# Optimization experiments

Hardware: AMD Instinct MI355X
Metric: run time of the kernel (lower is better)

Reference implementation:

```python
import jax, jax.numpy as jnp
import numpy as np

N = 100000
E = 3200000
F_IN = 256
F_OUT = 256
HID = 64


def setup_inputs() -> dict:
    key = jax.random.key(0)
    ks = jax.random.split(key, 16)
    stdv = 1.0 / np.sqrt(F_OUT)
    std_att = 1.0 / np.sqrt(HID)
    std_att_vec = 1.0 / np.sqrt(3.0)
    u = lambda k, shape, s: jax.random.uniform(k, shape, jnp.float32, -s, s)
    return {
        "inputx": jax.random.normal(ks[0], (N, F_IN), jnp.float32),
        "row_A": jax.random.randint(ks[1], (E,), 0, N),
        "col_A": jax.random.randint(ks[2], (E,), 0, N),
        "val_A": jax.random.uniform(ks[3], (E,), jnp.float32),
        "row_A2": jax.random.randint(ks[4], (E,), 0, N),
        "col_A2": jax.random.randint(ks[5], (E,), 0, N),
        "val_A2": jax.random.uniform(ks[6], (E,), jnp.float32),
        "weight_A": u(ks[7], (F_IN, F_OUT), stdv),
        "weight_A2": u(ks[8], (F_IN, F_OUT), stdv),
        "weight_mlp": u(ks[9], (F_IN, F_OUT), stdv),
        "W_k0": u(ks[10], (F_OUT, HID), std_att),
        "W_k1": u(ks[11], (F_OUT, HID), std_att),
        "W_k2": u(ks[12], (F_OUT, HID), std_att),
        "att_vec_A": u(ks[13], (F_OUT, HID), std_att),
        "att_vec_A2": u(ks[14], (F_OUT, HID), std_att),
        "att_vec_mlp": u(ks[15], (F_OUT, HID), std_att),
        "att_vec": u(jax.random.fold_in(key, 99), (3, 3), std_att_vec),
    }


def _spmm(row, col, val, x, n):
    # COO sparse-dense matmul: out[r] += val_e * x[c]
    return jax.ops.segment_sum(val[:, None] * x[col], row, num_segments=n)


def reference(inputx, row_A, col_A, val_A, row_A2, col_A2, val_A2,
              weight_A, weight_A2, weight_mlp, W_k0, W_k1, W_k2,
              att_vec_A, att_vec_A2, att_vec_mlp, att_vec):
    n = inputx.shape[0]
    out_A = jax.nn.relu(_spmm(row_A, col_A, val_A, inputx @ weight_A, n))
    out_A2 = jax.nn.relu(_spmm(row_A2, col_A2, val_A2, inputx @ weight_A2, n))
    out_mlp = jax.nn.relu(inputx @ weight_mlp)
    # attention gating
    T = 3.0
    k0 = jnp.mean(out_A @ W_k0, axis=0, keepdims=True)    # [1, HID]
    k1 = jnp.mean(out_A2 @ W_k1, axis=0, keepdims=True)
    k2 = jnp.mean(out_mlp @ W_k2, axis=0, keepdims=True)
    logits = jnp.concatenate([
        (out_A @ att_vec_A) @ k0.T,      # [N, 1]
        (out_A2 @ att_vec_A2) @ k1.T,
        (out_mlp @ att_vec_mlp) @ k2.T,
    ], axis=1)                           # [N, 3]
    att = jax.nn.softmax((jax.nn.sigmoid(logits) @ att_vec) / T, axis=1)
    return 3.0 * (att[:, 0:1] * out_A + att[:, 1:2] * out_A2 + att[:, 2:3] * out_mlp)
```

## Files before the change

### kernel.cpp

```cpp
#include <hip/hip_runtime.h>

typedef __bf16 bf16;
typedef __bf16 bf16x4 __attribute__((ext_vector_type(4)));
typedef __bf16 bf16x8 __attribute__((ext_vector_type(8)));
typedef float f32x4 __attribute__((ext_vector_type(4)));

__device__ __forceinline__ f32x4 bf2f(bf16x4 v){
  f32x4 r; r[0]=(float)v[0]; r[1]=(float)v[1]; r[2]=(float)v[2]; r[3]=(float)v[3]; return r;
}

#define NBMAX 1600
#define NBP   1601
#define CHUNK 16384

__global__ __launch_bounds__(256) void k_xcvt(const float* __restrict__ X, bf16* __restrict__ Xb, int total){
  int i = (blockIdx.x*256 + threadIdx.x)*8;
  if (i + 8 <= total){
    float4 a = *(const float4*)(X+i);
    float4 b = *(const float4*)(X+i+4);
    bf16x8 v;
    v[0]=(bf16)a.x; v[1]=(bf16)a.y; v[2]=(bf16)a.z; v[3]=(bf16)a.w;
    v[4]=(bf16)b.x; v[5]=(bf16)b.y; v[6]=(bf16)b.z; v[7]=(bf16)b.w;
    *(bf16x8*)(Xb+i) = v;
  }
}

__global__ __launch_bounds__(256) void k_wt(const float* __restrict__ W0, const float* __restrict__ W1,
                                            const float* __restrict__ W2, bf16* __restrict__ WT3){
  int n = blockIdx.x, mat = blockIdx.y, k = threadIdx.x;
  const float* W = (mat==0)?W0:((mat==1)?W1:W2);
  WT3[mat*65536 + n*256 + k] = (bf16)W[k*256 + n];
}

__global__ __launch_bounds__(512) void k_gemm(const bf16* __restrict__ Xb, const bf16* __restrict__ WT3,
        bf16* __restrict__ O0, bf16* __restrict__ O1, bf16* __restrict__ O2,
        float* __restrict__ colsum, int N){
  __shared__ __align__(16) bf16 sA[128*32];
  __shared__ __align__(16) bf16 sB[256*32];
  __shared__ float gcs[256];
  int t = threadIdx.x;
  int lane = t & 63, wave = t>>6, wm = wave>>2, wn = wave&3;
  int mat = blockIdx.y;
  int m0 = blockIdx.x*128;
  const bf16* WT = WT3 + mat*65536;
  bf16* OUT = (mat==0)?O0:((mat==1)?O1:O2);

  f32x4 acc[4][4];
#pragma unroll
  for (int i=0;i<4;i++)
#pragma unroll
    for (int j=0;j<4;j++){ acc[i][j][0]=0.f; acc[i][j][1]=0.f; acc[i][j][2]=0.f; acc[i][j][3]=0.f; }

  int ar = t>>2, ac = t&3;
  int alc = ac ^ ((ar>>1)&3);
  int agrow = m0 + ar; if (agrow > N-1) agrow = N-1;
  const bf16* gA = Xb + (size_t)agrow*256 + alc*8;
  bf16* lA = sA + ar*32 + ac*8;

  int br = t>>2, bc = t&3;
  int blc = bc ^ ((br>>1)&3);
  const bf16* gB0 = WT + br*256 + blc*8;
  const bf16* gB1 = WT + (br+128)*256 + blc*8;
  bf16* lB0 = sB + br*32 + bc*8;
  bf16* lB1 = sB + (br+128)*32 + bc*8;

  for (int k0=0; k0<256; k0+=32){
    __syncthreads();
    *(bf16x8*)lA  = *(const bf16x8*)(gA  + k0);
    *(bf16x8*)lB0 = *(const bf16x8*)(gB0 + k0);
    *(bf16x8*)lB1 = *(const bf16x8*)(gB1 + k0);
    __syncthreads();

    bf16x8 af[4], bfr[4];
#pragma unroll
    for (int i=0;i<4;i++){
      int arow = wm*64 + i*16 + (lane&15);
      int pc = (lane>>4) ^ ((arow>>1)&3);
      af[i] = *(const bf16x8*)(sA + arow*32 + pc*8);
    }
#pragma unroll
    for (int j=0;j<4;j++){
      int brow = wn*64 + j*16 + (lane&15);
      int pc = (lane>>4) ^ ((brow>>1)&3);
      bfr[j] = *(const bf16x8*)(sB + brow*32 + pc*8);
    }
#pragma unroll
    for (int i=0;i<4;i++)
#pragma unroll
      for (int j=0;j<4;j++)
        acc[i][j] = __builtin_amdgcn_mfma_f32_16x16x32_bf16(af[i], bfr[j], acc[i][j], 0,0,0);
  }

  int col0 = wn*64 + (lane&15);
  int rb = m0 + wm*64 + ((lane>>4)<<2);
  bool isrelu = (mat==2);
  float pj[4] = {0.f,0.f,0.f,0.f};
#pragma unroll
  for (int i=0;i<4;i++){
#pragma unroll
    for (int tt=0; tt<4; tt++){
      int r = rb + i*16 + tt;
      if (r < N){
#pragma unroll
        for (int j=0;j<4;j++){
          float vv = acc[i][j][tt];
          if (isrelu && vv < 0.f) vv = 0.f;
          if (isrelu) pj[j] += vv;
          OUT[(size_t)r*256 + col0 + j*16] = (bf16)vv;
        }
      }
    }
  }
  if (isrelu){
    if (t < 256) gcs[t] = 0.f;
    __syncthreads();
#pragma unroll
    for (int j=0;j<4;j++) atomicAdd(&gcs[col0 + j*16], pj[j]);
    __syncthreads();
    if (t < 256) atomicAdd(&colsum[512 + t], gcs[t]);
  }
}

__global__ __launch_bounds__(512) void k_bcnt(const int* __restrict__ rowA, const int* __restrict__ rowA2,
    int* __restrict__ bcnt, int E, int NB){
  __shared__ int hist[NBMAX];
  int mat = blockIdx.y;
  const int* row = mat? rowA2 : rowA;
  int t = threadIdx.x;
  for (int i=t; i<NB; i+=512) hist[i] = 0;
  __syncthreads();
  int base = blockIdx.x * CHUNK;
  int endi = base + CHUNK; if (endi > E) endi = E;
  for (int i = base + t; i < endi; i += 512) atomicAdd(&hist[row[i] >> 6], 1);
  __syncthreads();
  for (int i=t; i<NB; i+=512){
    int c = hist[i];
    if (c) atomicAdd(&bcnt[mat*NBMAX + i], c);
  }
}

__global__ __launch_bounds__(256) void k_bscan(const int* __restrict__ bcnt, int* __restrict__ gstart,
    int* __restrict__ gcur, int NB, int E){
  __shared__ int ss[256];
  __shared__ int carry;
  int mat = blockIdx.x;
  int t = threadIdx.x;
  if (t==0) carry = 0;
  __syncthreads();
  for (int base=0; base<NB; base+=256){
    int i = base + t;
    int v = (i < NB) ? bcnt[mat*NBMAX + i] : 0;
    ss[t] = v; __syncthreads();
    for (int off=1; off<256; off<<=1){
      int u = (t>=off)? ss[t-off] : 0;
      __syncthreads();
      ss[t] += u;
      __syncthreads();
    }
    int excl = carry + ss[t] - v;
    if (i < NB){ gstart[mat*NBP + i] = excl; gcur[mat*NB + i] = excl; }
    int tot = ss[255];
    __syncthreads();
    if (t==0) carry += tot;
    __syncthreads();
  }
  if (t==0) gstart[mat*NBP + NB] = E;
}

__global__ __launch_bounds__(512) void k_binT(const int* __restrict__ rowA, const int* __restrict__ colA,
    const float* __restrict__ valA, const int* __restrict__ rowA2, const int* __restrict__ colA2,
    const float* __restrict__ valA2, int* __restrict__ gcur,
    int2* __restrict__ pTA, int2* __restrict__ pTA2, int E, int NB){
  __shared__ int hist[NBMAX];
  int mat = blockIdx.y;
  const int* row = mat? rowA2 : rowA;
  const int* col = mat? colA2 : colA;
  const float* val = mat? valA2 : valA;
  int2* pT = mat? pTA2 : pTA;
  int t = threadIdx.x;
  for (int i=t; i<NB; i+=512) hist[i] = 0;
  __syncthreads();
  int base = blockIdx.x * CHUNK;
  int endi = base + CHUNK; if (endi > E) endi = E;
  for (int i = base + t; i < endi; i += 512) atomicAdd(&hist[row[i] >> 6], 1);
  __syncthreads();
  for (int i=t; i<NB; i+=512){
    int c = hist[i];
    if (c) hist[i] = atomicAdd(&gcur[mat*NB + i], c);
  }
  __syncthreads();
  for (int i = base + t; i < endi; i += 512){
    int r = row[i];
    int pos = atomicAdd(&hist[r >> 6], 1);
    int2 p; p.x = ((r & 63) << 17) | col[i]; p.y = __float_as_int(val[i]);
    pT[pos] = p;
  }
}

__global__ __launch_bounds__(256) void k_csr(const int2* __restrict__ pTA, const int2* __restrict__ pTA2,
    const int* __restrict__ gstart, int* __restrict__ rsA, int* __restrict__ rsA2,
    int2* __restrict__ permA, int2* __restrict__ permA2, int N, int NB, int E){
  __shared__ int rowst[64];
  __shared__ int fill[64];
  int mat = blockIdx.y;
  const int2* pT = mat? pTA2 : pTA;
  int2* perm = mat? permA2 : permA;
  int* rs = mat? rsA2 : rsA;
  int b = blockIdx.x;
  int t = threadIdx.x;
  int r0 = b*64;
  int start = gstart[mat*NBP + b];
  int end   = gstart[mat*NBP + b + 1];
  if (t < 64) fill[t] = 0;
  __syncthreads();
  for (int i = start + t; i < end; i += 256) atomicAdd(&fill[pT[i].x >> 17], 1);
  __syncthreads();
  if (t < 64){
    int v = fill[t];
    int x = v;
#pragma unroll
    for (int off=1; off<64; off<<=1){
      int u = __shfl_up(x, off, 64);
      if (t >= off) x += u;
    }
    int st = start + x - v;
    rowst[t] = st;
    if (r0 + t < N) rs[r0 + t] = st;
    fill[t] = 0;
  }
  __syncthreads();
  for (int i = start + t; i < end; i += 256){
    int2 e = pT[i];
    int rl = e.x >> 17;
    int pos = atomicAdd(&fill[rl], 1);
    int2 o; o.x = e.x & 0x1FFFF; o.y = e.y;
    perm[rowst[rl] + pos] = o;
  }
  if (t == 0 && b == NB-1) rs[N] = E;
}

__global__ __launch_bounds__(256) void k_spmm(const bf16* __restrict__ XA, const bf16* __restrict__ XA2,
    const int* __restrict__ rsA, const int* __restrict__ rsA2,
    const int2* __restrict__ permA, const int2* __restrict__ permA2,
    bf16* __restrict__ outA, bf16* __restrict__ outA2, float* __restrict__ colsum, int N){
  __shared__ float scs[1024];
  int mat = blockIdx.y;
  const bf16* src = mat? XA2 : XA;
  const int* rs = mat? rsA2 : rsA;
  const int2* perm = mat? permA2 : permA;
  bf16* dst = mat? outA2 : outA;
  int t = threadIdx.x, lane = t & 63, wv = t >> 6;
  int c = lane*4;
  int r0 = blockIdx.x*64;
  f32x4 csum; csum[0]=0.f; csum[1]=0.f; csum[2]=0.f; csum[3]=0.f;

  for (int rr = wv; rr < 64; rr += 4){
    int row = r0 + rr;
    if (row >= N) break;
    int e = rs[row], eend = rs[row+1];
    f32x4 acc; acc[0]=0.f; acc[1]=0.f; acc[2]=0.f; acc[3]=0.f;

    int2 p0, p1, p2, p3;
    bool have = (e + 3 < eend);
    if (have){ p0 = perm[e]; p1 = perm[e+1]; p2 = perm[e+2]; p3 = perm[e+3]; }
    while (have){
      bf16x4 g0 = *(const bf16x4*)(src + (size_t)p0.x*256 + c);
      bf16x4 g1 = *(const bf16x4*)(src + (size_t)p1.x*256 + c);
      bf16x4 g2 = *(const bf16x4*)(src + (size_t)p2.x*256 + c);
      bf16x4 g3 = *(const bf16x4*)(src + (size_t)p3.x*256 + c);
      float v0 = __int_as_float(p0.y), v1 = __int_as_float(p1.y);
      float v2 = __int_as_float(p2.y), v3 = __int_as_float(p3.y);
      e += 4;
      have = (e + 3 < eend);
      if (have){ p0 = perm[e]; p1 = perm[e+1]; p2 = perm[e+2]; p3 = perm[e+3]; }
      acc += v0 * bf2f(g0);
      acc += v1 * bf2f(g1);
      acc += v2 * bf2f(g2);
      acc += v3 * bf2f(g3);
    }
    for (; e < eend; ++e){
      int2 p = perm[e];
      acc += __int_as_float(p.y) * bf2f(*(const bf16x4*)(src + (size_t)p.x*256 + c));
    }
    bf16x4 o;
#pragma unroll
    for (int k=0;k<4;k++){
      float v = acc[k] < 0.f ? 0.f : acc[k];
      o[k] = (bf16)v;
      csum[k] += v;
    }
    *(bf16x4*)(dst + (size_t)row*256 + c) = o;
  }

#pragma unroll
  for (int k=0;k<4;k++) scs[wv*256 + c + k] = csum[k];
  __syncthreads();
  if (wv == 0){
#pragma unroll
    for (int k=0;k<4;k++){
      float s = scs[c+k] + scs[256+c+k] + scs[512+c+k] + scs[768+c+k];
      atomicAdd(&colsum[mat*256 + c + k], s);
    }
  }
}

__global__ void k_attn(const float* __restrict__ colsum,
    const float* __restrict__ Wk0, const float* __restrict__ Wk1, const float* __restrict__ Wk2,
    const float* __restrict__ V0, const float* __restrict__ V1, const float* __restrict__ V2,
    float* __restrict__ wvec, int N){
  __shared__ float smean[768];
  __shared__ float sk[192];
  int t = threadIdx.x;
  float invN = 1.f/(float)N;
  smean[t]     = colsum[t]     * invN;
  smean[t+256] = colsum[t+256] * invN;
  smean[t+512] = colsum[t+512] * invN;
  __syncthreads();
  if (t < 192){
    int j = t>>6, h = t&63;
    const float* Wk = (j==0)?Wk0:((j==1)?Wk1:Wk2);
    float s = 0.f;
    for (int cc=0; cc<256; cc++) s += smean[j*256+cc]*Wk[cc*64+h];
    sk[j*64+h] = s;
  }
  __syncthreads();
  int c = t;
  for (int j=0;j<3;j++){
    const float* V = (j==0)?V0:((j==1)?V1:V2);
    float s = 0.f;
    for (int h=0;h<64;h++) s += V[c*64+h]*sk[j*64+h];
    wvec[j*256+c] = s;
  }
}

__global__ __launch_bounds__(256) void k_epi(const bf16* __restrict__ A, const bf16* __restrict__ B,
    const bf16* __restrict__ M, const float* __restrict__ wvec, const float* __restrict__ av9,
    float* __restrict__ out, int N){
  __shared__ float sw[768];
  __shared__ float sav[9];
  int t = threadIdx.x;
  sw[t] = wvec[t]; sw[t+256] = wvec[t+256]; sw[t+512] = wvec[t+512];
  if (t < 9) sav[t] = av9[t];
  __syncthreads();
  int row = blockIdx.x*4 + (t>>6);
  if (row >= N) return;
  int lane = t & 63;
  int c = lane*4;
  f32x4 a = bf2f(*(const bf16x4*)(A + (size_t)row*256 + c));
  f32x4 b = bf2f(*(const bf16x4*)(B + (size_t)row*256 + c));
  f32x4 m = bf2f(*(const bf16x4*)(M + (size_t)row*256 + c));
  float p0 = a[0]*sw[c] + a[1]*sw[c+1] + a[2]*sw[c+2] + a[3]*sw[c+3];
  float p1 = b[0]*sw[256+c] + b[1]*sw[256+c+1] + b[2]*sw[256+c+2] + b[3]*sw[256+c+3];
  float p2 = m[0]*sw[512+c] + m[1]*sw[512+c+1] + m[2]*sw[512+c+2] + m[3]*sw[512+c+3];
#pragma unroll
  for (int off=32; off>=1; off>>=1){
    p0 += __shfl_xor(p0, off);
    p1 += __shfl_xor(p1, off);
    p2 += __shfl_xor(p2, off);
  }
  float s0 = 1.f/(1.f+expf(-p0));
  float s1 = 1.f/(1.f+expf(-p1));
  float s2 = 1.f/(1.f+expf(-p2));
  float g0 = (s0*sav[0] + s1*sav[3] + s2*sav[6]) * (1.f/3.f);
  float g1 = (s0*sav[1] + s1*sav[4] + s2*sav[7]) * (1.f/3.f);
  float g2 = (s0*sav[2] + s1*sav[5] + s2*sav[8]) * (1.f/3.f);
  float mx = fmaxf(g0, fmaxf(g1,g2));
  float e0 = expf(g0-mx), e1 = expf(g1-mx), e2 = expf(g2-mx);
  float inv = 3.f/(e0+e1+e2);
  float a0 = e0*inv, a1 = e1*inv, a2 = e2*inv;
  f32x4 o = a0*a + a1*b + a2*m;
  *(f32x4*)(out + (size_t)row*256 + c) = o;
}

extern "C" void kernel_launch(void* const* d_in, const int* in_sizes, int n_in,
                              void* d_out, int out_size, void* d_ws, size_t ws_size,
                              hipStream_t stream){
  const float* X    = (const float*)d_in[0];
  const int*   rowA = (const int*)d_in[1];
  const int*   colA = (const int*)d_in[2];
  const float* valA = (const float*)d_in[3];
  const int*   rowA2= (const int*)d_in[4];
  const int*   colA2= (const int*)d_in[5];
  const float* valA2= (const float*)d_in[6];
  const float* W0   = (const float*)d_in[7];
  const float* W1   = (const float*)d_in[8];
  const float* W2   = (const float*)d_in[9];
  const float* Wk0  = (const float*)d_in[10];
  const float* Wk1  = (const float*)d_in[11];
  const float* Wk2  = (const float*)d_in[12];
  const float* V0   = (const float*)d_in[13];
  const float* V1   = (const float*)d_in[14];
  const float* V2   = (const float*)d_in[15];
  const float* AV9  = (const float*)d_in[16];
  int N = in_sizes[0] / 256;
  int E = in_sizes[1];
  int NB = (N + 63) >> 6;

  char* ws = (char*)d_ws;
  size_t off = 0;
  auto take = [&](size_t b)->char*{ char* r = ws + off; off = (off + b + 255) & ~(size_t)255; return r; };
  size_t mb = (size_t)N*256*2;
  bf16* WT3    = (bf16*)take((size_t)3*256*256*2);
  bf16* XbOutA = (bf16*)take(mb);
  bf16* XAb    = (bf16*)take(mb);
  bf16* XA2b   = (bf16*)take(mb);
  bf16* XMb    = (bf16*)take(mb);
  bf16* outA2b = (bf16*)take(mb);
  int* rsA    = (int*)take((size_t)(N+1)*4);
  int* rsA2   = (int*)take((size_t)(N+1)*4);
  int* gcur   = (int*)take((size_t)2*NB*4);
  int* bcnt   = (int*)take((size_t)2*NBMAX*4);
  int* gstart = (int*)take((size_t)2*NBP*4);
  float* colsum = (float*)take(768*4);
  float* wvec   = (float*)take(768*4);
  int2* permA  = (int2*)take((size_t)E*8);
  int2* permA2 = (int2*)take((size_t)E*8);
  int2* pTA  = (int2*)XbOutA;
  int2* pTA2 = pTA + E;

  hipMemsetAsync(bcnt, 0, (size_t)2*NBMAX*4, stream);
  hipMemsetAsync(colsum, 0, 768*4, stream);

  int total = N*256;
  k_xcvt<<<dim3((total/8 + 255)/256),256,0,stream>>>(X, XbOutA, total);
  k_wt<<<dim3(256,3),256,0,stream>>>(W0,W1,W2,WT3);
  k_gemm<<<dim3((N+127)/128,3),512,0,stream>>>(XbOutA, WT3, XAb, XA2b, XMb, colsum, N);
  int ebl2 = (E + CHUNK-1)/CHUNK;
  k_bcnt<<<dim3(ebl2,2),512,0,stream>>>(rowA,rowA2,bcnt,E,NB);
  k_bscan<<<2,256,0,stream>>>(bcnt,gstart,gcur,NB,E);
  k_binT<<<dim3(ebl2,2),512,0,stream>>>(rowA,colA,valA,rowA2,colA2,valA2,gcur,pTA,pTA2,E,NB);
  k_csr<<<dim3(NB,2),256,0,stream>>>(pTA,pTA2,gstart,rsA,rsA2,permA,permA2,N,NB,E);
  k_spmm<<<dim3(NB,2),256,0,stream>>>(XAb,XA2b,rsA,rsA2,permA,permA2,XbOutA,outA2b,colsum,N);
  k_attn<<<1,256,0,stream>>>(colsum,Wk0,Wk1,Wk2,V0,V1,V2,wvec,N);
  k_epi<<<dim3((N+3)/4),256,0,stream>>>(XbOutA,outA2b,XMb,wvec,AV9,(float*)d_out,N);
}
```

Baseline: 1.179 ms.

## Cache per-chunk histograms, shrink SpMM blocks to four rows, reorder GEMM grid

The row histogram computed in k_bcnt is now written out per chunk, so k_binT reads it back instead of recounting rows. k_spmm now launches one block per four rows instead of per 64 rows, which gives far more blocks for load balance. Its column sums go to eight striped partial buffers to reduce atomic contention, and k_attn reduces those partials. The GEMM grid puts the matrix index on x so the three weight matrices share each X tile in cache. The cost is extra global histogram storage and many more SpMM blocks, each doing its own reduction and atomics.

```diff
diff --git a/kernel.cpp b/kernel.cpp
--- a/kernel.cpp
+++ b/kernel.cpp
@@ -40,8 +40,8 @@
   __shared__ float gcs[256];
   int t = threadIdx.x;
   int lane = t & 63, wave = t>>6, wm = wave>>2, wn = wave&3;
-  int mat = blockIdx.y;
-  int m0 = blockIdx.x*128;
+  int mat = blockIdx.x;
+  int m0 = blockIdx.y*128;
   const bf16* WT = WT3 + mat*65536;
   bf16* OUT = (mat==0)?O0:((mat==1)?O1:O2);
 
@@ -122,7 +122,7 @@
 }
 
 __global__ __launch_bounds__(512) void k_bcnt(const int* __restrict__ rowA, const int* __restrict__ rowA2,
-    int* __restrict__ bcnt, int E, int NB){
+    int* __restrict__ bcnt, int* __restrict__ chist, int E, int NB){
   __shared__ int hist[NBMAX];
   int mat = blockIdx.y;
   const int* row = mat? rowA2 : rowA;
@@ -133,8 +133,10 @@
   int endi = base + CHUNK; if (endi > E) endi = E;
   for (int i = base + t; i < endi; i += 512) atomicAdd(&hist[row[i] >> 6], 1);
   __syncthreads();
+  int* ch = chist + ((size_t)(mat*gridDim.x + blockIdx.x))*NBMAX;
   for (int i=t; i<NB; i+=512){
     int c = hist[i];
+    ch[i] = c;
     if (c) atomicAdd(&bcnt[mat*NBMAX + i], c);
   }
 }
@@ -169,7 +171,7 @@
 
 __global__ __launch_bounds__(512) void k_binT(const int* __restrict__ rowA, const int* __restrict__ colA,
     const float* __restrict__ valA, const int* __restrict__ rowA2, const int* __restrict__ colA2,
-    const float* __restrict__ valA2, int* __restrict__ gcur,
+    const float* __restrict__ valA2, int* __restrict__ gcur, const int* __restrict__ chist,
     int2* __restrict__ pTA, int2* __restrict__ pTA2, int E, int NB){
   __shared__ int hist[NBMAX];
   int mat = blockIdx.y;
@@ -178,17 +180,16 @@
   const float* val = mat? valA2 : valA;
   int2* pT = mat? pTA2 : pTA;
   int t = threadIdx.x;
-  for (int i=t; i<NB; i+=512) hist[i] = 0;
-  __syncthreads();
-  int base = blockIdx.x * CHUNK;
-  int endi = base + CHUNK; if (endi > E) endi = E;
-  for (int i = base + t; i < endi; i += 512) atomicAdd(&hist[row[i] >> 6], 1);
+  const int* ch = chist + ((size_t)(mat*gridDim.x + blockIdx.x))*NBMAX;
+  for (int i=t; i<NB; i+=512) hist[i] = ch[i];
   __syncthreads();
   for (int i=t; i<NB; i+=512){
     int c = hist[i];
     if (c) hist[i] = atomicAdd(&gcur[mat*NB + i], c);
   }
   __syncthreads();
+  int base = blockIdx.x * CHUNK;
+  int endi = base + CHUNK; if (endi > E) endi = E;
   for (int i = base + t; i < endi; i += 512){
     int r = row[i];
     int pos = atomicAdd(&hist[r >> 6], 1);
@@ -242,7 +243,7 @@
 __global__ __launch_bounds__(256) void k_spmm(const bf16* __restrict__ XA, const bf16* __restrict__ XA2,
     const int* __restrict__ rsA, const int* __restrict__ rsA2,
     const int2* __restrict__ permA, const int2* __restrict__ permA2,
-    bf16* __restrict__ outA, bf16* __restrict__ outA2, float* __restrict__ colsum, int N){
+    bf16* __restrict__ outA, bf16* __restrict__ outA2, float* __restrict__ part, int N){
   __shared__ float scs[1024];
   int mat = blockIdx.y;
   const bf16* src = mat? XA2 : XA;
@@ -251,12 +252,10 @@
   bf16* dst = mat? outA2 : outA;
   int t = threadIdx.x, lane = t & 63, wv = t >> 6;
   int c = lane*4;
-  int r0 = blockIdx.x*64;
-  f32x4 csum; csum[0]=0.f; csum[1]=0.f; csum[2]=0.f; csum[3]=0.f;
-
-  for (int rr = wv; rr < 64; rr += 4){
-    int row = r0 + rr;
-    if (row >= N) break;
+  int row = blockIdx.x*4 + wv;
+  f32x4 outv; outv[0]=0.f; outv[1]=0.f; outv[2]=0.f; outv[3]=0.f;
+
+  if (row < N){
     int e = rs[row], eend = rs[row+1];
     f32x4 acc; acc[0]=0.f; acc[1]=0.f; acc[2]=0.f; acc[3]=0.f;
 
@@ -287,24 +286,25 @@
     for (int k=0;k<4;k++){
       float v = acc[k] < 0.f ? 0.f : acc[k];
       o[k] = (bf16)v;
-      csum[k] += v;
+      outv[k] = v;
     }
     *(bf16x4*)(dst + (size_t)row*256 + c) = o;
   }
 
 #pragma unroll
-  for (int k=0;k<4;k++) scs[wv*256 + c + k] = csum[k];
+  for (int k=0;k<4;k++) scs[wv*256 + c + k] = outv[k];
   __syncthreads();
   if (wv == 0){
+    float* pp = part + ((blockIdx.x & 7)*2 + mat)*256;
 #pragma unroll
     for (int k=0;k<4;k++){
       float s = scs[c+k] + scs[256+c+k] + scs[512+c+k] + scs[768+c+k];
-      atomicAdd(&colsum[mat*256 + c + k], s);
-    }
-  }
-}
-
-__global__ void k_attn(const float* __restrict__ colsum,
+      atomicAdd(&pp[c+k], s);
+    }
+  }
+}
+
+__global__ void k_attn(const float* __restrict__ colsum, const float* __restrict__ part,
     const float* __restrict__ Wk0, const float* __restrict__ Wk1, const float* __restrict__ Wk2,
     const float* __restrict__ V0, const float* __restrict__ V1, const float* __restrict__ V2,
     float* __restrict__ wvec, int N){
@@ -312,9 +312,15 @@
   __shared__ float sk[192];
   int t = threadIdx.x;
   float invN = 1.f/(float)N;
-  smean[t]     = colsum[t]     * invN;
-  smean[t+256] = colsum[t+256] * invN;
-  smean[t+512] = colsum[t+512] * invN;
+  float s0 = 0.f, s1 = 0.f;
+#pragma unroll
+  for (int s=0; s<8; s++){
+    s0 += part[(s*2+0)*256 + t];
+    s1 += part[(s*2+1)*256 + t];
+  }
+  smean[t]     = s0 * invN;
+  smean[t+256] = s1 * invN;
+  smean[t+512] = colsum[512+t] * invN;
   __syncthreads();
   if (t < 192){
     int j = t>>6, h = t&63;
@@ -395,6 +401,7 @@
   int N = in_sizes[0] / 256;
   int E = in_sizes[1];
   int NB = (N + 63) >> 6;
+  int ebl2 = (E + CHUNK-1)/CHUNK;
 
   char* ws = (char*)d_ws;
   size_t off = 0;
@@ -411,7 +418,9 @@
   int* gcur   = (int*)take((size_t)2*NB*4);
   int* bcnt   = (int*)take((size_t)2*NBMAX*4);
   int* gstart = (int*)take((size_t)2*NBP*4);
+  int* chist  = (int*)take((size_t)2*ebl2*NBMAX*4);
   float* colsum = (float*)take(768*4);
+  float* part   = (float*)take((size_t)8*2*256*4);
   float* wvec   = (float*)take(768*4);
   int2* permA  = (int2*)take((size_t)E*8);
   int2* permA2 = (int2*)take((size_t)E*8);
@@ -420,17 +429,17 @@
 
   hipMemsetAsync(bcnt, 0, (size_t)2*NBMAX*4, stream);
   hipMemsetAsync(colsum, 0, 768*4, stream);
+  hipMemsetAsync(part, 0, (size_t)8*2*256*4, stream);
 
   int total = N*256;
   k_xcvt<<<dim3((total/8 + 255)/256),256,0,stream>>>(X, XbOutA, total);
   k_wt<<<dim3(256,3),256,0,stream>>>(W0,W1,W2,WT3);
-  k_gemm<<<dim3((N+127)/128,3),512,0,stream>>>(XbOutA, WT3, XAb, XA2b, XMb, colsum, N);
-  int ebl2 = (E + CHUNK-1)/CHUNK;
-  k_bcnt<<<dim3(ebl2,2),512,0,stream>>>(rowA,rowA2,bcnt,E,NB);
+  k_gemm<<<dim3(3,(N+127)/128),512,0,stream>>>(XbOutA, WT3, XAb, XA2b, XMb, colsum, N);
+  k_bcnt<<<dim3(ebl2,2),512,0,stream>>>(rowA,rowA2,bcnt,chist,E,NB);
   k_bscan<<<2,256,0,stream>>>(bcnt,gstart,gcur,NB,E);
-  k_binT<<<dim3(ebl2,2),512,0,stream>>>(rowA,colA,valA,rowA2,colA2,valA2,gcur,pTA,pTA2,E,NB);
+  k_binT<<<dim3(ebl2,2),512,0,stream>>>(rowA,colA,valA,rowA2,colA2,valA2,gcur,chist,pTA,pTA2,E,NB);
   k_csr<<<dim3(NB,2),256,0,stream>>>(pTA,pTA2,gstart,rsA,rsA2,permA,permA2,N,NB,E);
-  k_spmm<<<dim3(NB,2),256,0,stream>>>(XAb,XA2b,rsA,rsA2,permA,permA2,XbOutA,outA2b,colsum,N);
-  k_attn<<<1,256,0,stream>>>(colsum,Wk0,Wk1,Wk2,V0,V1,V2,wvec,N);
+  k_spmm<<<dim3((N+3)/4,2),256,0,stream>>>(XAb,XA2b,rsA,rsA2,permA,permA2,XbOutA,outA2b,part,N);
+  k_attn<<<1,256,0,stream>>>(colsum,part,Wk0,Wk1,Wk2,V0,V1,V2,wvec,N);
   k_epi<<<dim3((N+3)/4),256,0,stream>>>(XbOutA,outA2b,XMb,wvec,AV9,(float*)d_out,N);
 }
```

After: 1.257 ms. 1.07x slower.
